# Optimization experiments

Measured on AMD Instinct MI355X. Metric: run time of the kernel, lower is better.

The kernel has to match this reference:

```python
import jax, jax.numpy as jnp
import numpy as np

BIG_CONST = 1000000.0
LN_EPS = 1e-5

B, S, D = 2, 1024, 1024
N, H = 16, D // 16            # n_head, d_head
POS_LEN = 2 * S - 1


def setup_inputs() -> dict:
    key = jax.random.key(0)
    ks = jax.random.split(key, 16)
    std_qkv = np.sqrt(1.0 / float(D + N * H))   # EinsumLayer init: 1/sqrt(fan_in+fan_out)
    std_post = np.sqrt(1.0 / float(N * H + D))
    return {
        "q": jax.random.normal(ks[0], (B, S, D), jnp.float32),
        "k": jax.random.normal(ks[1], (B, S, D), jnp.float32),
        "v": jax.random.normal(ks[2], (B, S, D), jnp.float32),
        "pos_enc": jax.random.normal(ks[3], (POS_LEN, D), jnp.float32),
        "attn_mask": jax.random.randint(ks[4], (B, 1, 1, S), 0, 2, jnp.int32),
        "q_w": jax.random.normal(ks[5], (D, N, H), jnp.float32) * std_qkv,
        "k_w": jax.random.normal(ks[6], (D, N, H), jnp.float32) * std_qkv,
        "k_b": jnp.zeros((N, H), jnp.float32),
        "v_w": jax.random.normal(ks[7], (D, N, H), jnp.float32) * std_qkv,
        "v_b": jnp.zeros((N, H), jnp.float32),
        "r_w_bias": jax.random.uniform(ks[8], (N, 1, H), jnp.float32, 0.0, 0.1),
        "r_r_bias": jax.random.uniform(ks[9], (N, 1, H), jnp.float32, 0.0, 0.1),
        "r_kernel": jax.random.uniform(ks[10], (N, D, H), jnp.float32, 0.0, 0.1),
        "post_w": jax.random.normal(ks[11], (N, H, D), jnp.float32) * std_post,
        "post_b": jnp.zeros((D,), jnp.float32),
        "ln_g": jnp.ones((D,), jnp.float32),
        "ln_b": jnp.zeros((D,), jnp.float32),
    }


def reference(q, k, v, pos_enc, attn_mask, q_w, k_w, k_b, v_w, v_b,
              r_w_bias, r_r_bias, r_kernel, post_w, post_b, ln_g, ln_b):
    input_q = q
    d_head = q_w.shape[-1]
    normalizer = 1.0 / np.sqrt(d_head)

    # head projections -> [B, N, L, H]
    qh = jnp.einsum('bld,dnh->bnlh', q, q_w)
    kh = jnp.einsum('bld,dnh->bnlh', k, k_w) + k_b[None, :, None, :] * 0 + jnp.transpose(k_b, (0, 1))[None, :, None, :] * 0 + k_b.reshape(1, k_b.shape[0], 1, k_b.shape[1])
    kh = jnp.einsum('bld,dnh->bnlh', k, k_w) + k_b.reshape(1, -1, 1, d_head)
    vh = jnp.einsum('bld,dnh->bnlh', v, v_w) + v_b.reshape(1, -1, 1, d_head)

    # content score: (q + r_w_bias) @ k^T * normalizer   [B,N,S,S]
    content = jnp.einsum('bnqh,bnkh->bnqk', qh + r_w_bias[None], kh) * normalizer

    # positional term (rel_shift with shift=0): r = pos_enc @ r_kernel -> [N, P, H]
    r = jnp.einsum('pd,ndh->nph', pos_enc, r_kernel)
    pos_scores = jnp.einsum('bnqh,nph->bnqp', qh + r_r_bias[None], r) * normalizer
    # shift=0 => reshape-swap + narrow + reshape-back is an exact identity; then narrow to k_len
    k_len = kh.shape[-2]
    pos_term = pos_scores[..., :k_len]

    attn_score = (content + pos_term).astype(jnp.float32)
    attn_score = attn_score - BIG_CONST * attn_mask.astype(jnp.float32)
    attn_dist = jax.nn.softmax(attn_score, axis=-1)

    out = jnp.einsum('bnqk,bnkh->bnqh', attn_dist, vh)          # [B,N,S,H]
    attn_out = jnp.einsum('bnlh,nhd->bld', out, post_w) + post_b

    x = input_q + attn_out
    mu = jnp.mean(x, axis=-1, keepdims=True)
    var = jnp.mean(jnp.square(x - mu), axis=-1, keepdims=True)
    return (x - mu) / jnp.sqrt(var + LN_EPS) * ln_g + ln_b
```

## Files before the change

kernel.cpp:

```cpp
#include <hip/hip_runtime.h>
#include <cstddef>
#include <cstdint>

typedef unsigned short u16;
typedef unsigned int   u32;

#define S_LEN  1024
#define NHEAD  16
#define HDIM   64
#define DMODEL 1024
#define NORMSC 0.125f
#define BIGC   1000000.0f
#define LOG2E  1.44269504088896f
#define SC2    (0.125f * 1.44269504088896f)

typedef __bf16 bf16x8 __attribute__((ext_vector_type(8)));
typedef float  f32x4  __attribute__((ext_vector_type(4)));

#define MFMA16(a, b, c) __builtin_amdgcn_mfma_f32_16x16x32_bf16((a), (b), (c), 0, 0, 0)

__device__ __forceinline__ u16 f2bf(float f) {
    u32 u = __float_as_uint(f);
    u32 r = (u + 0x7fffu + ((u >> 16) & 1u)) >> 16;
    return (u16)r;
}

__device__ __forceinline__ void async16(const void* g, void* l) {
    __builtin_amdgcn_global_load_lds(
        (__attribute__((address_space(1))) void*)(g),
        (__attribute__((address_space(3))) void*)(l), 16, 0, 0);
}

__global__ __launch_bounds__(256) void prep_all(
    const float* q, const float* k, const float* v, const float* pos,
    const float* qw, const float* kw, const float* vw, const float* pw, const float* rk,
    u16* qbf, u16* kbf, u16* vbf, u16* posb,
    u16* qwT, u16* kwT, u16* vwT, u16* pwT, u16* WrT)
{
    __shared__ float tb[32][33];
    const int bid = blockIdx.x, tid = threadIdx.x;
    if (bid < 7168) {
        const float* s; u16* d; int base;
        if (bid < 2048)      { s = q;   d = qbf;  base = bid; }
        else if (bid < 4096) { s = k;   d = kbf;  base = bid - 2048; }
        else if (bid < 6144) { s = v;   d = vbf;  base = bid - 4096; }
        else                 { s = pos; d = posb; base = bid - 6144; }
        const int i = base * 1024 + tid * 4;
        const float4 val = *(const float4*)&s[i];
        uint2 o;
        o.x = (u32)f2bf(val.x) | ((u32)f2bf(val.y) << 16);
        o.y = (u32)f2bf(val.z) | ((u32)f2bf(val.w) << 16);
        *(uint2*)&d[i] = o;
        return;
    }
    const int t = bid - 7168;
    const float* in; u16* out; int ild, r0, c0;
    if (t < 4096) {
        const int ts = t & 1023;
        if (t < 1024)      { in = qw; out = qwT; }
        else if (t < 2048) { in = kw; out = kwT; }
        else if (t < 3072) { in = vw; out = vwT; }
        else               { in = pw; out = pwT; }
        ild = 1024;
        r0 = (ts >> 5) * 32; c0 = (ts & 31) * 32;
    } else {
        const int ts = t - 4096;
        const int n = ts >> 6, tt = ts & 63;
        in = rk + (size_t)n * 65536; out = WrT + (size_t)n * 65536;
        ild = 64;
        r0 = (tt >> 1) * 32; c0 = (tt & 1) * 32;
    }
    const int tx = tid & 31, ty = tid >> 5;
    for (int i = ty; i < 32; i += 8)
        tb[i][tx] = in[(size_t)(r0 + i) * ild + c0 + tx];
    __syncthreads();
    for (int i = ty; i < 32; i += 8)
        out[(size_t)(c0 + i) * 1024 + r0 + tx] = f2bf(tb[tx][i]);
}

struct GB {
    const u16* A; const u16* Bt; const float* bias;
    void* C; int M; int mode; int kr0; int kr1;
};

__global__ __launch_bounds__(256) void gemm_mfma(GB g0, GB g1, GB g2, GB g3)
{
    GB g;
    switch (blockIdx.z) { case 0: g = g0; break; case 1: g = g1; break;
                          case 2: g = g2; break; default: g = g3; }
    const int bm = blockIdx.y * 128;
    if (bm >= g.M) return;
    const int bn = blockIdx.x * 128;
    __shared__ u16 As[4096];
    __shared__ u16 Bs[4096];
    const int tid = threadIdx.x;
    const int w = tid >> 6, lane = tid & 63;
    const int wm = (w >> 1) * 64, wn = (w & 1) * 64;
    const int l15 = lane & 15, l16 = lane >> 4;
    f32x4 acc[4][4] = {};
    const char* Ab = (const char*)g.A;
    const char* Bb = (const char*)g.Bt;
    for (int k0 = g.kr0; k0 < g.kr1; k0 += 32) {
        __syncthreads();
#pragma unroll
        for (int i = 0; i < 2; ++i) {
            const int m = (i * 4 + w) * 1024 + lane * 16;
            const int r = m >> 6, cb = m & 63;
            async16(Ab + ((size_t)(bm + r) * 1024 + k0) * 2 + cb, (char*)As + m);
            async16(Bb + ((size_t)(bn + r) * 1024 + k0) * 2 + cb, (char*)Bs + m);
        }
        __syncthreads();
        bf16x8 af[4], bfr[4];
#pragma unroll
        for (int i = 0; i < 4; ++i)
            af[i] = *(const bf16x8*)&As[(wm + i * 16 + l15) * 32 + l16 * 8];
#pragma unroll
        for (int j = 0; j < 4; ++j)
            bfr[j] = *(const bf16x8*)&Bs[(wn + j * 16 + l15) * 32 + l16 * 8];
#pragma unroll
        for (int i = 0; i < 4; ++i)
#pragma unroll
            for (int j = 0; j < 4; ++j)
                acc[i][j] = MFMA16(af[i], bfr[j], acc[i][j]);
    }
#pragma unroll
    for (int i = 0; i < 4; ++i) {
#pragma unroll
        for (int j = 0; j < 4; ++j) {
            const int c = bn + wn + j * 16 + l15;
            const float bv = g.bias ? g.bias[c] : 0.0f;
#pragma unroll
            for (int rg = 0; rg < 4; ++rg) {
                const int m = bm + wm + i * 16 + l16 * 4 + rg;
                float v = acc[i][j][rg] + bv;
                if (g.mode == 1) {
                    const int b2 = m >> 10, l = m & 1023, n = c >> 6, h = c & 63;
                    ((float*)g.C)[(((size_t)(b2 * NHEAD + n)) * 1024 + l) * 64 + h] = v;
                } else if (g.mode == 2) {
                    const int n = c >> 6, h = c & 63;
                    ((float*)g.C)[((size_t)n * 1024 + m) * 64 + h] = v;
                } else if (g.mode == 3) {
                    const int b2 = m >> 10, l = m & 1023, n = c >> 6, h = c & 63;
                    ((u16*)g.C)[(((size_t)(b2 * NHEAD + n)) * 1024 + l) * 64 + h] = f2bf(v);
                } else {
                    ((float*)g.C)[(size_t)m * 1024 + c] = v;
                }
            }
        }
    }
}

__global__ __launch_bounds__(256) void prep2(
    const float* kh, const float* r, const float* rwb, const float* rrb,
    const int* mask, const float* vh, u16* keff, float* cc, u16* vT)
{
    __shared__ float tb[32][33];
    const int bid = blockIdx.x, tid = threadIdx.x;
    if (bid < 2048) {
        const int t = bid * 256 + tid;
        const int row = t >> 4, li = t & 15;
        const int n = (row >> 10) & 15, k = row & 1023, b = row >> 14;
        const float4 kv = *(const float4*)&kh[(size_t)row * 64 + li * 4];
        const float4 rv = *(const float4*)&r[((size_t)n * 1024 + k) * 64 + li * 4];
        const float4 w1 = *(const float4*)&rwb[n * 64 + li * 4];
        const float4 w2 = *(const float4*)&rrb[n * 64 + li * 4];
        float s = w1.x * kv.x + w1.y * kv.y + w1.z * kv.z + w1.w * kv.w
                + w2.x * rv.x + w2.y * rv.y + w2.z * rv.z + w2.w * rv.w;
        uint2 o;
        o.x = (u32)f2bf(kv.x + rv.x) | ((u32)f2bf(kv.y + rv.y) << 16);
        o.y = (u32)f2bf(kv.z + rv.z) | ((u32)f2bf(kv.w + rv.w) << 16);
        *(uint2*)&keff[(size_t)row * 64 + li * 4] = o;
#pragma unroll
        for (int m = 1; m < 16; m <<= 1) s += __shfl_xor(s, m);
        if (li == 0)
            cc[row] = LOG2E * (NORMSC * s - BIGC * (float)mask[b * 1024 + k]);
        return;
    }
    const int t = bid - 2048;
    const int n = t >> 6, tt = t & 63;
    const float* in = vh + (size_t)n * 65536;
    u16* out = vT + (size_t)n * 65536;
    const int r0 = (tt >> 1) * 32, c0 = (tt & 1) * 32;
    const int tx = tid & 31, ty = tid >> 5;
    for (int i = ty; i < 32; i += 8)
        tb[i][tx] = in[(size_t)(r0 + i) * 64 + c0 + tx];
    __syncthreads();
    for (int i = ty; i < 32; i += 8)
        out[(size_t)(c0 + i) * 1024 + r0 + tx] = f2bf(tb[tx][i]);
}

__global__ __launch_bounds__(128) void attn_mfma(
    const u16* qb, const u16* kb, const u16* vtb, const float* ccomb, u16* O)
{
    __shared__ u16   Ks[8192];
    __shared__ u16   Vs[8192];
    __shared__ __bf16 Ps[2][2048];
    const int tid = threadIdx.x;
    const int w = tid >> 6, lane = tid & 63;
    const int l15 = lane & 15, l16 = lane >> 4;
    const int head = blockIdx.x >> 5;
    const int q0 = (blockIdx.x & 31) * 32;
    const int b = head >> 4, n = head & 15;
    const size_t hoff = (size_t)head * 65536;
    const u16* qh = qb + hoff;
    const char* khc = (const char*)(kb + hoff);
    const char* vtc = (const char*)(vtb + hoff);
    const float* cc = ccomb + head * 1024;
    __bf16* Pw = Ps[w];

    bf16x8 qf[2];
    {
        const size_t rb = ((size_t)(q0 + w * 16 + l15)) * 64 + l16 * 8;
        qf[0] = *(const bf16x8*)&qh[rb];
        qf[1] = *(const bf16x8*)&qh[rb + 32];
    }
    f32x4 Oacc[4] = {};
    float lsum[4] = {};

    for (int kc = 0; kc < 8; ++kc) {
        __syncthreads();
#pragma unroll
        for (int i = 0; i < 8; ++i) {
            const int r = w * 64 + i * 8 + (lane >> 3);
            const int c = lane & 7;
            async16(khc + kc * 16384 + r * 128 + (((c + r) & 7) << 4),
                    (char*)Ks + (w * 64 + i * 8) * 128 + lane * 16);
        }
#pragma unroll
        for (int i = 0; i < 8; ++i) {
            const int r = w * 32 + i * 4 + (lane >> 4);
            const int c = lane & 15;
            async16(vtc + (size_t)r * 2048 + kc * 256 + (((c + r) & 15) << 4),
                    (char*)Vs + (w * 32 + i * 4) * 256 + lane * 16);
        }
        __syncthreads();

        f32x4 sc[8];
#pragma unroll
        for (int j = 0; j < 8; ++j) {
            const int rk = j * 16 + l15;
            const int base = rk * 64;
            f32x4 a = {0.f, 0.f, 0.f, 0.f};
            a = MFMA16(qf[0], *(const bf16x8*)&Ks[base + (((l16 - rk) & 7) << 3)], a);
            a = MFMA16(qf[1], *(const bf16x8*)&Ks[base + (((l16 + 4 - rk) & 7) << 3)], a);
            const float cadd = cc[kc * 128 + j * 16 + l15];
            sc[j] = a * SC2 + cadd;
        }
#pragma unroll
        for (int j = 0; j < 8; ++j) {
            const int cg = j * 2 + (l15 >> 3);
#pragma unroll
            for (int rg = 0; rg < 4; ++rg) {
                const float p = exp2f(sc[j][rg]);
                lsum[rg] += p;
                const int row = l16 * 4 + rg;
                Pw[row * 128 + (((cg - row) & 15) << 3) + (l15 & 7)] = (__bf16)p;
            }
        }
        bf16x8 pf[4];
#pragma unroll
        for (int f = 0; f < 4; ++f)
            pf[f] = *(const bf16x8*)&Pw[l15 * 128 + (((f * 4 + l16 - l15) & 15) << 3)];
#pragma unroll
        for (int t4 = 0; t4 < 4; ++t4) {
#pragma unroll
            for (int f = 0; f < 4; ++f) {
                const int r = t4 * 16 + l15;
                const bf16x8 vf = *(const bf16x8*)&Vs[r * 128 + (((f * 4 + l16 - r) & 15) << 3)];
                Oacc[t4] = MFMA16(pf[f], vf, Oacc[t4]);
            }
        }
    }
    float inv[4];
#pragma unroll
    for (int rg = 0; rg < 4; ++rg) {
        float s = lsum[rg];
#pragma unroll
        for (int m = 1; m < 16; m <<= 1) s += __shfl_xor(s, m);
        inv[rg] = 1.0f / s;
    }
#pragma unroll
    for (int t4 = 0; t4 < 4; ++t4) {
#pragma unroll
        for (int rg = 0; rg < 4; ++rg) {
            const int srow = q0 + w * 16 + l16 * 4 + rg;
            const int col = n * 64 + t4 * 16 + l15;
            O[((size_t)b * 1024 + srow) * 1024 + col] = f2bf(Oacc[t4][rg] * inv[rg]);
        }
    }
}

__global__ __launch_bounds__(256) void ln_kernel(
    const float* __restrict__ p0, const float* __restrict__ p1,
    const float* __restrict__ resid, const float* __restrict__ pb,
    const float* __restrict__ g, const float* __restrict__ bb,
    float* __restrict__ out)
{
    const int row = blockIdx.x;
    const int tid = threadIdx.x;
    const size_t i = (size_t)row * DMODEL + tid * 4;
    const float4 a  = *(const float4*)&p0[i];
    const float4 b2 = *(const float4*)&p1[i];
    const float4 r  = *(const float4*)&resid[i];
    const float4 pv = *(const float4*)&pb[tid * 4];
    float4 v;
    v.x = a.x + b2.x + r.x + pv.x;
    v.y = a.y + b2.y + r.y + pv.y;
    v.z = a.z + b2.z + r.z + pv.z;
    v.w = a.w + b2.w + r.w + pv.w;
    float s1 = v.x + v.y + v.z + v.w;
    float s2 = v.x * v.x + v.y * v.y + v.z * v.z + v.w * v.w;
#pragma unroll
    for (int off = 32; off; off >>= 1) {
        s1 += __shfl_down(s1, off);
        s2 += __shfl_down(s2, off);
    }
    __shared__ float rb[8];
    if ((tid & 63) == 0) { rb[tid >> 6] = s1; rb[4 + (tid >> 6)] = s2; }
    __syncthreads();
    if (tid == 0) {
        rb[0] = rb[0] + rb[1] + rb[2] + rb[3];
        rb[4] = rb[4] + rb[5] + rb[6] + rb[7];
    }
    __syncthreads();
    s1 = rb[0]; s2 = rb[4];
    const float mu = s1 * (1.0f / DMODEL);
    const float var = s2 * (1.0f / DMODEL) - mu * mu;
    const float rstd = rsqrtf(var + 1e-5f);
    const float4 gv = *(const float4*)&g[tid * 4];
    const float4 bv = *(const float4*)&bb[tid * 4];
    float4 o;
    o.x = (v.x - mu) * rstd * gv.x + bv.x;
    o.y = (v.y - mu) * rstd * gv.y + bv.y;
    o.z = (v.z - mu) * rstd * gv.z + bv.z;
    o.w = (v.w - mu) * rstd * gv.w + bv.w;
    *(float4*)&out[i] = o;
}

extern "C" void kernel_launch(void* const* d_in, const int* in_sizes, int n_in,
                              void* d_out, int out_size, void* d_ws, size_t ws_size,
                              hipStream_t stream)
{
    (void)in_sizes; (void)n_in; (void)out_size; (void)ws_size;
    const float* q   = (const float*)d_in[0];
    const float* k   = (const float*)d_in[1];
    const float* v   = (const float*)d_in[2];
    const float* pos = (const float*)d_in[3];
    const int*   msk = (const int*)d_in[4];
    const float* qw  = (const float*)d_in[5];
    const float* kw  = (const float*)d_in[6];
    const float* kbi = (const float*)d_in[7];
    const float* vw  = (const float*)d_in[8];
    const float* vbi = (const float*)d_in[9];
    const float* rwb = (const float*)d_in[10];
    const float* rrb = (const float*)d_in[11];
    const float* rk  = (const float*)d_in[12];
    const float* pw  = (const float*)d_in[13];
    const float* pb  = (const float*)d_in[14];
    const float* lg  = (const float*)d_in[15];
    const float* lb  = (const float*)d_in[16];
    float* out = (float*)d_out;

    float* ws  = (float*)d_ws;
    float* kh  = ws;
    float* vh  = kh + 2097152;
    float* rr  = vh + 2097152;
    float* cc  = rr + 1048576;
    u16* us    = (u16*)(cc + 32768);
    u16* qbf   = us;
    u16* kbf   = qbf + 2097152;
    u16* vbf   = kbf + 2097152;
    u16* posb  = vbf + 2097152;
    u16* qwT   = posb + 1048576;
    u16* kwT   = qwT + 1048576;
    u16* vwT   = kwT + 1048576;
    u16* WrT   = vwT + 1048576;
    u16* pwT   = WrT + 1048576;
    u16* qhb   = pwT + 1048576;
    u16* Obf   = qbf;
    u16* keffb = kbf;
    u16* vTb   = vbf;
    float* part0 = kh;
    float* part1 = vh;

    dim3 blk(256);
    prep_all<<<12288, blk, 0, stream>>>(q, k, v, pos, qw, kw, vw, pw, rk,
                                        qbf, kbf, vbf, posb, qwT, kwT, vwT, pwT, WrT);

    GB bq = {qbf,  qwT, nullptr, (void*)qhb, 2048, 3, 0, 1024};
    GB bk = {kbf,  kwT, kbi,     (void*)kh,  2048, 1, 0, 1024};
    GB bv = {vbf,  vwT, vbi,     (void*)vh,  2048, 1, 0, 1024};
    GB bp = {posb, WrT, nullptr, (void*)rr,  1024, 2, 0, 1024};
    gemm_mfma<<<dim3(8, 16, 4), blk, 0, stream>>>(bq, bk, bv, bp);

    prep2<<<4096, blk, 0, stream>>>(kh, rr, rwb, rrb, msk, vh, keffb, cc, vTb);

    attn_mfma<<<1024, dim3(128), 0, stream>>>(qhb, keffb, vTb, cc, Obf);

    GB bo0 = {Obf, pwT, nullptr, (void*)part0, 2048, 4, 0,   512};
    GB bo1 = {Obf, pwT, nullptr, (void*)part1, 2048, 4, 512, 1024};
    gemm_mfma<<<dim3(8, 16, 2), blk, 0, stream>>>(bo0, bo1, bo0, bo1);

    ln_kernel<<<2048, blk, 0, stream>>>(part0, part1, q, pb, lg, lb, out);
}
```

Baseline: 223.6 us.

## Split-K all projection GEMMs and attention keys, store bf16 partials, combine later

Every projection GEMM now runs as split-K: two halves for Q/K/V/pos and four quarters for the output projection. Each split writes bf16 partials in plain row-major layout, and prep2 and the layernorm kernel sum them and add the biases. Attention now uses 256-thread blocks over 64 queries each and splits the key range in two, writing unnormalised fp32 outputs plus row sums that a new comb_o kernel merges and normalises. The aim is more blocks for better CU occupancy and simpler GEMM epilogues. The cost is extra partial-buffer traffic, one more kernel launch, and added bf16 rounding of the partial sums.

After: 226.5 us. Within noise of the previous version (+1.3%).

```diff
diff --git a/kernel.cpp b/kernel.cpp
--- a/kernel.cpp
+++ b/kernel.cpp
@@ -24,7 +24,15 @@
     u32 r = (u + 0x7fffu + ((u >> 16) & 1u)) >> 16;
     return (u16)r;
 }
-
+__device__ __forceinline__ float bf2f(u32 v) {
+    return __uint_as_float(v << 16);
+}
+__device__ __forceinline__ float4 unp4(uint2 u) {
+    float4 f;
+    f.x = bf2f(u.x & 0xffffu); f.y = bf2f(u.x >> 16);
+    f.z = bf2f(u.y & 0xffffu); f.w = bf2f(u.y >> 16);
+    return f;
+}
 __device__ __forceinline__ void async16(const void* g, void* l) {
     __builtin_amdgcn_global_load_lds(
         (__attribute__((address_space(1))) void*)(g),
@@ -78,16 +86,18 @@
         out[(size_t)(c0 + i) * 1024 + r0 + tx] = f2bf(tb[tx][i]);
 }
 
-struct GB {
-    const u16* A; const u16* Bt; const float* bias;
-    void* C; int M; int mode; int kr0; int kr1;
-};
-
-__global__ __launch_bounds__(256) void gemm_mfma(GB g0, GB g1, GB g2, GB g3)
-{
-    GB g;
-    switch (blockIdx.z) { case 0: g = g0; break; case 1: g = g1; break;
-                          case 2: g = g2; break; default: g = g3; }
+struct GJ { const u16* A; const u16* Bt; u16* C; int M; int k0; int klen; };
+
+__global__ __launch_bounds__(256) void gemm_p(
+    GJ j0, GJ j1, GJ j2, GJ j3, GJ j4, GJ j5, GJ j6, GJ j7)
+{
+    GJ g;
+    switch (blockIdx.z) {
+        case 0: g = j0; break; case 1: g = j1; break;
+        case 2: g = j2; break; case 3: g = j3; break;
+        case 4: g = j4; break; case 5: g = j5; break;
+        case 6: g = j6; break; default: g = j7;
+    }
     const int bm = blockIdx.y * 128;
     if (bm >= g.M) return;
     const int bn = blockIdx.x * 128;
@@ -100,7 +110,8 @@
     f32x4 acc[4][4] = {};
     const char* Ab = (const char*)g.A;
     const char* Bb = (const char*)g.Bt;
-    for (int k0 = g.kr0; k0 < g.kr1; k0 += 32) {
+    const int kend = g.k0 + g.klen;
+    for (int k0 = g.k0; k0 < kend; k0 += 32) {
         __syncthreads();
 #pragma unroll
         for (int i = 0; i < 2; ++i) {
@@ -124,44 +135,42 @@
                 acc[i][j] = MFMA16(af[i], bfr[j], acc[i][j]);
     }
 #pragma unroll
-    for (int i = 0; i < 4; ++i) {
+    for (int i = 0; i < 4; ++i)
 #pragma unroll
         for (int j = 0; j < 4; ++j) {
             const int c = bn + wn + j * 16 + l15;
-            const float bv = g.bias ? g.bias[c] : 0.0f;
 #pragma unroll
             for (int rg = 0; rg < 4; ++rg) {
                 const int m = bm + wm + i * 16 + l16 * 4 + rg;
-                float v = acc[i][j][rg] + bv;
-                if (g.mode == 1) {
-                    const int b2 = m >> 10, l = m & 1023, n = c >> 6, h = c & 63;
-                    ((float*)g.C)[(((size_t)(b2 * NHEAD + n)) * 1024 + l) * 64 + h] = v;
-                } else if (g.mode == 2) {
-                    const int n = c >> 6, h = c & 63;
-                    ((float*)g.C)[((size_t)n * 1024 + m) * 64 + h] = v;
-                } else if (g.mode == 3) {
-                    const int b2 = m >> 10, l = m & 1023, n = c >> 6, h = c & 63;
-                    ((u16*)g.C)[(((size_t)(b2 * NHEAD + n)) * 1024 + l) * 64 + h] = f2bf(v);
-                } else {
-                    ((float*)g.C)[(size_t)m * 1024 + c] = v;
-                }
+                g.C[(size_t)m * 1024 + c] = f2bf(acc[i][j][rg]);
             }
         }
-    }
 }
 
 __global__ __launch_bounds__(256) void prep2(
-    const float* kh, const float* r, const float* rwb, const float* rrb,
-    const int* mask, const float* vh, u16* keff, float* cc, u16* vT)
+    const u16* pk0, const u16* pk1, const u16* pr0, const u16* pr1,
+    const u16* pv0, const u16* pv1, const u16* pq0, const u16* pq1,
+    const float* kbi, const float* vbi, const float* rwb, const float* rrb,
+    const int* mask, u16* keff, float* cc, u16* vT, u16* qhb)
 {
     __shared__ float tb[32][33];
     const int bid = blockIdx.x, tid = threadIdx.x;
     if (bid < 2048) {
         const int t = bid * 256 + tid;
         const int row = t >> 4, li = t & 15;
-        const int n = (row >> 10) & 15, k = row & 1023, b = row >> 14;
-        const float4 kv = *(const float4*)&kh[(size_t)row * 64 + li * 4];
-        const float4 rv = *(const float4*)&r[((size_t)n * 1024 + k) * 64 + li * 4];
+        const int n = (row >> 10) & 15, kk = row & 1023, b = row >> 14;
+        const size_t mi = ((size_t)(b * 1024 + kk)) * 1024 + n * 64 + li * 4;
+        const size_t pi = ((size_t)kk) * 1024 + n * 64 + li * 4;
+        const float4 k0v = unp4(*(const uint2*)&pk0[mi]);
+        const float4 k1v = unp4(*(const uint2*)&pk1[mi]);
+        const float4 r0v = unp4(*(const uint2*)&pr0[pi]);
+        const float4 r1v = unp4(*(const uint2*)&pr1[pi]);
+        const float4 kb4 = *(const float4*)&kbi[n * 64 + li * 4];
+        float4 kv, rv;
+        kv.x = k0v.x + k1v.x + kb4.x; kv.y = k0v.y + k1v.y + kb4.y;
+        kv.z = k0v.z + k1v.z + kb4.z; kv.w = k0v.w + k1v.w + kb4.w;
+        rv.x = r0v.x + r1v.x; rv.y = r0v.y + r1v.y;
+        rv.z = r0v.z + r1v.z; rv.w = r0v.w + r1v.w;
         const float4 w1 = *(const float4*)&rwb[n * 64 + li * 4];
         const float4 w2 = *(const float4*)&rrb[n * 64 + li * 4];
         float s = w1.x * kv.x + w1.y * kv.y + w1.z * kv.z + w1.w * kv.w
@@ -173,39 +182,60 @@
 #pragma unroll
         for (int m = 1; m < 16; m <<= 1) s += __shfl_xor(s, m);
         if (li == 0)
-            cc[row] = LOG2E * (NORMSC * s - BIGC * (float)mask[b * 1024 + k]);
+            cc[row] = LOG2E * (NORMSC * s - BIGC * (float)mask[b * 1024 + kk]);
         return;
     }
-    const int t = bid - 2048;
-    const int n = t >> 6, tt = t & 63;
-    const float* in = vh + (size_t)n * 65536;
-    u16* out = vT + (size_t)n * 65536;
-    const int r0 = (tt >> 1) * 32, c0 = (tt & 1) * 32;
-    const int tx = tid & 31, ty = tid >> 5;
-    for (int i = ty; i < 32; i += 8)
-        tb[i][tx] = in[(size_t)(r0 + i) * 64 + c0 + tx];
-    __syncthreads();
-    for (int i = ty; i < 32; i += 8)
-        out[(size_t)(c0 + i) * 1024 + r0 + tx] = f2bf(tb[tx][i]);
-}
-
-__global__ __launch_bounds__(128) void attn_mfma(
-    const u16* qb, const u16* kb, const u16* vtb, const float* ccomb, u16* O)
+    if (bid < 4096) {
+        const int t = bid - 2048;
+        const int head = t >> 6, tt = t & 63;
+        const int b = head >> 4, n = head & 15;
+        const int r0 = (tt >> 1) * 32, c0 = (tt & 1) * 32;
+        const int tx = tid & 31, ty = tid >> 5;
+        const float vb = vbi[n * 64 + c0 + tx];
+        for (int i = ty; i < 32; i += 8) {
+            const size_t idx = ((size_t)(b * 1024 + r0 + i)) * 1024 + n * 64 + c0 + tx;
+            tb[i][tx] = bf2f(pv0[idx]) + bf2f(pv1[idx]) + vb;
+        }
+        __syncthreads();
+        u16* out = vT + (size_t)head * 65536;
+        for (int i = ty; i < 32; i += 8)
+            out[(size_t)(c0 + i) * 1024 + r0 + tx] = f2bf(tb[tx][i]);
+        return;
+    }
+    const int t = bid - 4096;
+    const int e = t * 1024 + tid * 4;
+    const int m = e >> 10, c = e & 1023;
+    const float4 a = unp4(*(const uint2*)&pq0[e]);
+    const float4 b4 = unp4(*(const uint2*)&pq1[e]);
+    uint2 o;
+    o.x = (u32)f2bf(a.x + b4.x) | ((u32)f2bf(a.y + b4.y) << 16);
+    o.y = (u32)f2bf(a.z + b4.z) | ((u32)f2bf(a.w + b4.w) << 16);
+    const int b2 = m >> 10, l = m & 1023, n = c >> 6, h = c & 63;
+    *(uint2*)&qhb[(((size_t)(b2 * NHEAD + n)) * 1024 + l) * 64 + h] = o;
+}
+
+__global__ __launch_bounds__(256) void attn_mfma(
+    const u16* qb, const u16* kb, const u16* vtb, const float* ccomb,
+    float* o0, float* o1, float* lsb0, float* lsb1)
 {
     __shared__ u16   Ks[8192];
     __shared__ u16   Vs[8192];
-    __shared__ __bf16 Ps[2][2048];
+    __shared__ __bf16 Ps[4][1024];
     const int tid = threadIdx.x;
     const int w = tid >> 6, lane = tid & 63;
     const int l15 = lane & 15, l16 = lane >> 4;
-    const int head = blockIdx.x >> 5;
-    const int q0 = (blockIdx.x & 31) * 32;
+    const int ks = blockIdx.x >> 9;
+    const int r = blockIdx.x & 511;
+    const int head = r >> 4;
+    const int q0 = (r & 15) * 64;
     const int b = head >> 4, n = head & 15;
     const size_t hoff = (size_t)head * 65536;
     const u16* qh = qb + hoff;
     const char* khc = (const char*)(kb + hoff);
     const char* vtc = (const char*)(vtb + hoff);
     const float* cc = ccomb + head * 1024;
+    float* Op = ks ? o1 : o0;
+    float* ls = ks ? lsb1 : lsb0;
     __bf16* Pw = Ps[w];
 
     bf16x8 qf[2];
@@ -217,81 +247,98 @@
     f32x4 Oacc[4] = {};
     float lsum[4] = {};
 
-    for (int kc = 0; kc < 8; ++kc) {
+    for (int kc = ks * 4; kc < ks * 4 + 4; ++kc) {
         __syncthreads();
 #pragma unroll
-        for (int i = 0; i < 8; ++i) {
-            const int r = w * 64 + i * 8 + (lane >> 3);
-            const int c = lane & 7;
-            async16(khc + kc * 16384 + r * 128 + (((c + r) & 7) << 4),
-                    (char*)Ks + (w * 64 + i * 8) * 128 + lane * 16);
-        }
-#pragma unroll
-        for (int i = 0; i < 8; ++i) {
-            const int r = w * 32 + i * 4 + (lane >> 4);
-            const int c = lane & 15;
-            async16(vtc + (size_t)r * 2048 + kc * 256 + (((c + r) & 15) << 4),
-                    (char*)Vs + (w * 32 + i * 4) * 256 + lane * 16);
+        for (int i = 0; i < 4; ++i) {
+            const int m = (i * 4 + w) * 1024 + lane * 16;
+            const int kr = m >> 7, kcc = (m >> 4) & 7;
+            async16(khc + kc * 16384 + kr * 128 + (((kcc + kr) & 7) << 4), (char*)Ks + m);
+            const int vr = m >> 8, vc = (m >> 4) & 15;
+            async16(vtc + (size_t)vr * 2048 + kc * 256 + (((vc + vr) & 15) << 4), (char*)Vs + m);
         }
         __syncthreads();
 
         f32x4 sc[8];
 #pragma unroll
         for (int j = 0; j < 8; ++j) {
-            const int rk = j * 16 + l15;
-            const int base = rk * 64;
+            const int rk2 = j * 16 + l15;
+            const int base = rk2 * 64;
             f32x4 a = {0.f, 0.f, 0.f, 0.f};
-            a = MFMA16(qf[0], *(const bf16x8*)&Ks[base + (((l16 - rk) & 7) << 3)], a);
-            a = MFMA16(qf[1], *(const bf16x8*)&Ks[base + (((l16 + 4 - rk) & 7) << 3)], a);
+            a = MFMA16(qf[0], *(const bf16x8*)&Ks[base + (((l16 - rk2) & 7) << 3)], a);
+            a = MFMA16(qf[1], *(const bf16x8*)&Ks[base + (((l16 + 4 - rk2) & 7) << 3)], a);
             const float cadd = cc[kc * 128 + j * 16 + l15];
             sc[j] = a * SC2 + cadd;
         }
 #pragma unroll
-        for (int j = 0; j < 8; ++j) {
-            const int cg = j * 2 + (l15 >> 3);
-#pragma unroll
-            for (int rg = 0; rg < 4; ++rg) {
-                const float p = exp2f(sc[j][rg]);
-                lsum[rg] += p;
-                const int row = l16 * 4 + rg;
-                Pw[row * 128 + (((cg - row) & 15) << 3) + (l15 & 7)] = (__bf16)p;
+        for (int h2 = 0; h2 < 2; ++h2) {
+#pragma unroll
+            for (int j2 = 0; j2 < 4; ++j2) {
+                const int j = h2 * 4 + j2;
+                const int cg = j2 * 2 + (l15 >> 3);
+#pragma unroll
+                for (int rg = 0; rg < 4; ++rg) {
+                    const float p = exp2f(sc[j][rg]);
+                    lsum[rg] += p;
+                    const int row = l16 * 4 + rg;
+                    Pw[row * 64 + (((cg - row) & 7) << 3) + (l15 & 7)] = (__bf16)p;
+                }
             }
-        }
-        bf16x8 pf[4];
-#pragma unroll
-        for (int f = 0; f < 4; ++f)
-            pf[f] = *(const bf16x8*)&Pw[l15 * 128 + (((f * 4 + l16 - l15) & 15) << 3)];
-#pragma unroll
-        for (int t4 = 0; t4 < 4; ++t4) {
-#pragma unroll
-            for (int f = 0; f < 4; ++f) {
-                const int r = t4 * 16 + l15;
-                const bf16x8 vf = *(const bf16x8*)&Vs[r * 128 + (((f * 4 + l16 - r) & 15) << 3)];
-                Oacc[t4] = MFMA16(pf[f], vf, Oacc[t4]);
+            bf16x8 pf[2];
+#pragma unroll
+            for (int f = 0; f < 2; ++f)
+                pf[f] = *(const bf16x8*)&Pw[l15 * 64 + (((f * 4 + l16 - l15) & 7) << 3)];
+#pragma unroll
+            for (int t4 = 0; t4 < 4; ++t4) {
+#pragma unroll
+                for (int f = 0; f < 2; ++f) {
+                    const int vr = t4 * 16 + l15;
+                    const int ch = h2 * 8 + f * 4 + l16;
+                    const bf16x8 vf = *(const bf16x8*)&Vs[vr * 128 + (((ch - vr) & 15) << 3)];
+                    Oacc[t4] = MFMA16(pf[f], vf, Oacc[t4]);
+                }
             }
         }
     }
-    float inv[4];
-#pragma unroll
-    for (int rg = 0; rg < 4; ++rg) {
-        float s = lsum[rg];
-#pragma unroll
-        for (int m = 1; m < 16; m <<= 1) s += __shfl_xor(s, m);
-        inv[rg] = 1.0f / s;
-    }
-#pragma unroll
-    for (int t4 = 0; t4 < 4; ++t4) {
+#pragma unroll
+    for (int t4 = 0; t4 < 4; ++t4)
 #pragma unroll
         for (int rg = 0; rg < 4; ++rg) {
             const int srow = q0 + w * 16 + l16 * 4 + rg;
             const int col = n * 64 + t4 * 16 + l15;
-            O[((size_t)b * 1024 + srow) * 1024 + col] = f2bf(Oacc[t4][rg] * inv[rg]);
-        }
-    }
+            Op[((size_t)b * 1024 + srow) * 1024 + col] = Oacc[t4][rg];
+        }
+    float4 s4;
+#pragma unroll
+    for (int rg = 0; rg < 4; ++rg) {
+        float s = lsum[rg];
+#pragma unroll
+        for (int m = 1; m < 16; m <<= 1) s += __shfl_xor(s, m);
+        ((float*)&s4)[rg] = s;
+    }
+    if (l15 == 0)
+        *(float4*)&ls[head * 1024 + q0 + w * 16 + l16 * 4] = s4;
+}
+
+__global__ __launch_bounds__(256) void comb_o(
+    const float* o0, const float* o1, const float* ls0, const float* ls1, u16* Obf)
+{
+    const int i = (blockIdx.x * 256 + threadIdx.x) * 4;
+    const int row = i >> 10, col = i & 1023;
+    const int b = row >> 10, s = row & 1023, n = col >> 6;
+    const int head = b * 16 + n;
+    const float inv = 1.0f / (ls0[head * 1024 + s] + ls1[head * 1024 + s]);
+    const float4 a = *(const float4*)&o0[i];
+    const float4 c = *(const float4*)&o1[i];
+    uint2 o;
+    o.x = (u32)f2bf((a.x + c.x) * inv) | ((u32)f2bf((a.y + c.y) * inv) << 16);
+    o.y = (u32)f2bf((a.z + c.z) * inv) | ((u32)f2bf((a.w + c.w) * inv) << 16);
+    *(uint2*)&Obf[i] = o;
 }
 
 __global__ __launch_bounds__(256) void ln_kernel(
-    const float* __restrict__ p0, const float* __restrict__ p1,
+    const u16* __restrict__ p0, const u16* __restrict__ p1,
+    const u16* __restrict__ p2, const u16* __restrict__ p3,
     const float* __restrict__ resid, const float* __restrict__ pb,
     const float* __restrict__ g, const float* __restrict__ bb,
     float* __restrict__ out)
@@ -299,15 +346,17 @@
     const int row = blockIdx.x;
     const int tid = threadIdx.x;
     const size_t i = (size_t)row * DMODEL + tid * 4;
-    const float4 a  = *(const float4*)&p0[i];
-    const float4 b2 = *(const float4*)&p1[i];
-    const float4 r  = *(const float4*)&resid[i];
+    const float4 a0 = unp4(*(const uint2*)&p0[i]);
+    const float4 a1 = unp4(*(const uint2*)&p1[i]);
+    const float4 a2 = unp4(*(const uint2*)&p2[i]);
+    const float4 a3 = unp4(*(const uint2*)&p3[i]);
+    const float4 rr = *(const float4*)&resid[i];
     const float4 pv = *(const float4*)&pb[tid * 4];
     float4 v;
-    v.x = a.x + b2.x + r.x + pv.x;
-    v.y = a.y + b2.y + r.y + pv.y;
-    v.z = a.z + b2.z + r.z + pv.z;
-    v.w = a.w + b2.w + r.w + pv.w;
+    v.x = a0.x + a1.x + a2.x + a3.x + rr.x + pv.x;
+    v.y = a0.y + a1.y + a2.y + a3.y + rr.y + pv.y;
+    v.z = a0.z + a1.z + a2.z + a3.z + rr.z + pv.z;
+    v.w = a0.w + a1.w + a2.w + a3.w + rr.w + pv.w;
     float s1 = v.x + v.y + v.z + v.w;
     float s2 = v.x * v.x + v.y * v.y + v.z * v.z + v.w * v.w;
 #pragma unroll
@@ -361,45 +410,65 @@
     const float* lb  = (const float*)d_in[16];
     float* out = (float*)d_out;
 
-    float* ws  = (float*)d_ws;
-    float* kh  = ws;
-    float* vh  = kh + 2097152;
-    float* rr  = vh + 2097152;
-    float* cc  = rr + 1048576;
-    u16* us    = (u16*)(cc + 32768);
-    u16* qbf   = us;
-    u16* kbf   = qbf + 2097152;
-    u16* vbf   = kbf + 2097152;
-    u16* posb  = vbf + 2097152;
-    u16* qwT   = posb + 1048576;
-    u16* kwT   = qwT + 1048576;
-    u16* vwT   = kwT + 1048576;
-    u16* WrT   = vwT + 1048576;
-    u16* pwT   = WrT + 1048576;
-    u16* qhb   = pwT + 1048576;
-    u16* Obf   = qbf;
-    u16* keffb = kbf;
-    u16* vTb   = vbf;
-    float* part0 = kh;
-    float* part1 = vh;
+    float* fb = (float*)d_ws;
+    float* cc   = fb;
+    float* ls0  = cc + 32768;
+    float* ls1  = ls0 + 32768;
+    float* Op0  = ls1 + 32768;
+    float* Op1  = Op0 + 2097152;
+    u16* us   = (u16*)(Op1 + 2097152);
+    u16* qbf  = us;
+    u16* kbf  = qbf + 2097152;
+    u16* vbf  = kbf + 2097152;
+    u16* posb = vbf + 2097152;
+    u16* qwT  = posb + 1048576;
+    u16* kwT  = qwT + 1048576;
+    u16* vwT  = kwT + 1048576;
+    u16* pwT  = vwT + 1048576;
+    u16* WrT  = pwT + 1048576;
+    u16* qhb  = WrT + 1048576;
+    u16* keffb= qhb + 2097152;
+    u16* vTb  = keffb + 2097152;
+    u16* pq0  = vTb + 2097152;
+    u16* pq1  = pq0 + 2097152;
+    u16* pk0  = pq1 + 2097152;
+    u16* pk1  = pk0 + 2097152;
+    u16* pv0  = pk1 + 2097152;
+    u16* pv1  = pv0 + 2097152;
+    u16* pr0  = pv1 + 2097152;
+    u16* pr1  = pr0 + 1048576;
+    u16* po0  = pr1 + 1048576;
+    u16* po1  = po0 + 2097152;
+    u16* po2  = po1 + 2097152;
+    u16* po3  = po2 + 2097152;
+    u16* Obf  = qbf;
 
     dim3 blk(256);
     prep_all<<<12288, blk, 0, stream>>>(q, k, v, pos, qw, kw, vw, pw, rk,
                                         qbf, kbf, vbf, posb, qwT, kwT, vwT, pwT, WrT);
 
-    GB bq = {qbf,  qwT, nullptr, (void*)qhb, 2048, 3, 0, 1024};
-    GB bk = {kbf,  kwT, kbi,     (void*)kh,  2048, 1, 0, 1024};
-    GB bv = {vbf,  vwT, vbi,     (void*)vh,  2048, 1, 0, 1024};
-    GB bp = {posb, WrT, nullptr, (void*)rr,  1024, 2, 0, 1024};
-    gemm_mfma<<<dim3(8, 16, 4), blk, 0, stream>>>(bq, bk, bv, bp);
-
-    prep2<<<4096, blk, 0, stream>>>(kh, rr, rwb, rrb, msk, vh, keffb, cc, vTb);
-
-    attn_mfma<<<1024, dim3(128), 0, stream>>>(qhb, keffb, vTb, cc, Obf);
-
-    GB bo0 = {Obf, pwT, nullptr, (void*)part0, 2048, 4, 0,   512};
-    GB bo1 = {Obf, pwT, nullptr, (void*)part1, 2048, 4, 512, 1024};
-    gemm_mfma<<<dim3(8, 16, 2), blk, 0, stream>>>(bo0, bo1, bo0, bo1);
-
-    ln_kernel<<<2048, blk, 0, stream>>>(part0, part1, q, pb, lg, lb, out);
-}
+    GJ jq0 = {qbf,  qwT, pq0, 2048, 0,   512};
+    GJ jq1 = {qbf,  qwT, pq1, 2048, 512, 512};
+    GJ jk0 = {kbf,  kwT, pk0, 2048, 0,   512};
+    GJ jk1 = {kbf,  kwT, pk1, 2048, 512, 512};
+    GJ jv0 = {vbf,  vwT, pv0, 2048, 0,   512};
+    GJ jv1 = {vbf,  vwT, pv1, 2048, 512, 512};
+    GJ jp0 = {posb, WrT, pr0, 1024, 0,   512};
+    GJ jp1 = {posb, WrT, pr1, 1024, 512, 512};
+    gemm_p<<<dim3(8, 16, 8), blk, 0, stream>>>(jq0, jq1, jk0, jk1, jv0, jv1, jp0, jp1);
+
+    prep2<<<6144, blk, 0, stream>>>(pk0, pk1, pr0, pr1, pv0, pv1, pq0, pq1,
+                                    kbi, vbi, rwb, rrb, msk, keffb, cc, vTb, qhb);
+
+    attn_mfma<<<1024, blk, 0, stream>>>(qhb, keffb, vTb, cc, Op0, Op1, ls0, ls1);
+
+    comb_o<<<2048, blk, 0, stream>>>(Op0, Op1, ls0, ls1, Obf);
+
+    GJ jo0 = {Obf, pwT, po0, 2048, 0,   256};
+    GJ jo1 = {Obf, pwT, po1, 2048, 256, 256};
+    GJ jo2 = {Obf, pwT, po2, 2048, 512, 256};
+    GJ jo3 = {Obf, pwT, po3, 2048, 768, 256};
+    gemm_p<<<dim3(8, 16, 4), blk, 0, stream>>>(jo0, jo1, jo2, jo3, jo0, jo0, jo0, jo0);
+
+    ln_kernel<<<2048, blk, 0, stream>>>(po0, po1, po2, po3, q, pb, lg, lb, out);
+}
```
